# Performance work log

Hardware: AMD Instinct MI355X
Metric: run time of the kernel (lower is better)

The kernel has to match this reference:

```python
import jax, jax.numpy as jnp
import numpy as np

B, S, D = 512, 8, 1024
L = 6        # n_layers
LOOPS = 4    # n_loops
EPS = 1e-5   # LayerNorm eps (torch default)


def setup_inputs() -> dict:
    key = jax.random.key(0)
    ks = jax.random.split(key, 8)
    s = 1.0 / np.sqrt(D)  # torch Linear default init bound
    x = jax.random.normal(ks[0], (B, S, D), jnp.float32)
    gamma = jnp.ones((L, D), jnp.float32)
    beta = jnp.zeros((L, D), jnp.float32)
    Wg = jax.random.uniform(ks[1], (L, D, D), jnp.float32, -s, s)
    bg = jax.random.uniform(ks[2], (L, D), jnp.float32, -s, s)
    Wt = jax.random.uniform(ks[3], (L, D, D), jnp.float32, -s, s)
    bt = jax.random.uniform(ks[4], (L, D), jnp.float32, -s, s)
    Wc = jax.random.uniform(ks[5], (D, 1), jnp.float32, -s, s)
    bc = jax.random.uniform(ks[6], (1,), jnp.float32, -s, s)
    return {"x": x, "gamma": gamma, "beta": beta, "Wg": Wg, "bg": bg,
            "Wt": Wt, "bt": bt, "Wc": Wc, "bc": bc}


def _block(x, gamma, beta, Wg, bg, Wt, bt):
    # LayerNorm over last dim
    mu = jnp.mean(x, axis=-1, keepdims=True)
    var = jnp.mean(jnp.square(x - mu), axis=-1, keepdims=True)
    xn = (x - mu) * jax.lax.rsqrt(var + EPS) * gamma + beta
    g = jax.nn.sigmoid(jnp.einsum('bsd,de->bse', xn, Wg) + bg)
    t = jnp.tanh(jnp.einsum('bsd,de->bse', xn, Wt) + bt)
    return x * (1.0 - g) + t * g


def reference(x, gamma, beta, Wg, bg, Wt, bt, Wc, bc):
    confs = []
    for _ in range(LOOPS):
        for i in range(L):
            x = _block(x, gamma[i], beta[i], Wg[i], bg[i], Wt[i], bt[i])
        # confidence = sigmoid(Linear(x.mean(dim=1)))  -> (B, 1)
        confs.append(jax.nn.sigmoid(x.mean(axis=1) @ Wc + bc))
    return x, jnp.stack(confs)  # ((B,S,D), (LOOPS,B,1))
```

## Files before the change

### kernel.cpp

```cpp
#include <hip/hip_runtime.h>
#include <hip/hip_bf16.h>
#include <math.h>

#define B_ 512
#define S_ 8
#define D_ 1024
#define L_ 6
#define LOOPS_ 4
#define R_ (B_*S_)
#define LD_ (L_*D_)
#define EPSV 1e-5f

#define BM 128
#define BN 128
#define BK 64
#define NT (D_/BK)
#define TILE_USH 24576

typedef __attribute__((ext_vector_type(4))) float f32x4;
typedef __attribute__((ext_vector_type(8))) _Float16 f16x8;

__device__ __forceinline__ float bf2f(unsigned short u){
  union { float f; unsigned int i; } v; v.i = ((unsigned int)u) << 16; return v.f;
}
__device__ __forceinline__ unsigned short f2h(float f){
  _Float16 h = (_Float16)f;
  union { _Float16 h; unsigned short u; } v; v.h = h; return v.u;
}
__device__ __forceinline__ float loadf(const void* p, size_t i, int bf){
  return bf ? bf2f(((const unsigned short*)p)[i]) : ((const float*)p)[i];
}
__device__ __forceinline__ void gload16(const void* g, void* l){
  __builtin_amdgcn_global_load_lds((const __attribute__((address_space(1))) void*)g,
                                   (__attribute__((address_space(3))) void*)l, 16, 0, 0);
}

__global__ void k_detect(const unsigned int* __restrict__ gamma_raw, int* __restrict__ flag){
  if (threadIdx.x == 0 && blockIdx.x == 0)
    *flag = (gamma_raw[0] == 0x3F803F80u) ? 1 : 0;
}

__global__ void k_x2f(const void* __restrict__ x, float* __restrict__ xf,
                      const int* __restrict__ flag, int n4){
  int i = blockIdx.x * blockDim.x + threadIdx.x;
  if (i >= n4) return;
  if (*flag){
    ushort4 u = ((const ushort4*)x)[i];
    float4 f; f.x = bf2f(u.x); f.y = bf2f(u.y); f.z = bf2f(u.z); f.w = bf2f(u.w);
    ((float4*)xf)[i] = f;
  } else {
    ((float4*)xf)[i] = ((const float4*)x)[i];
  }
}

__global__ void k_small(const void* g, const void* b, const void* bgp, const void* btp,
                        const void* wcp, const void* bcp,
                        float* __restrict__ sm, const int* __restrict__ flag){
  int i = blockIdx.x * blockDim.x + threadIdx.x;
  int bf = *flag;
  if (i < LD_)               sm[i] = loadf(g,   i,          bf);
  else if (i < 2*LD_)        sm[i] = loadf(b,   i - LD_,    bf);
  else if (i < 3*LD_)        sm[i] = loadf(bgp, i - 2*LD_,  bf);
  else if (i < 4*LD_)        sm[i] = loadf(btp, i - 3*LD_,  bf);
  else if (i < 4*LD_ + D_)   sm[i] = loadf(wcp, i - 4*LD_,  bf);
  else if (i == 4*LD_ + D_)  sm[i] = loadf(bcp, 0,          bf);
}

__global__ void k_transpose(const void* __restrict__ Wg, const void* __restrict__ Wt,
                            ushort* __restrict__ WgT, ushort* __restrict__ WtT,
                            const int* __restrict__ flag){
  __shared__ ushort tile[32][33];
  int bf = *flag;
  int z = blockIdx.z;
  const void* src; ushort* dst;
  size_t base;
  if (z < L_) { src = Wg; dst = WgT + (size_t)z * D_ * D_;        base = (size_t)z * D_ * D_; }
  else        { src = Wt; dst = WtT + (size_t)(z - L_) * D_ * D_; base = (size_t)(z - L_) * D_ * D_; }
  int d0 = blockIdx.y * 32, e0 = blockIdx.x * 32;
  int tx = threadIdx.x, ty = threadIdx.y;
  #pragma unroll
  for (int i = 0; i < 4; i++){
    int r = ty + i * 8;
    size_t idx = base + (size_t)(d0 + r) * D_ + e0 + tx;
    float v = bf ? bf2f(((const ushort*)src)[idx]) : ((const float*)src)[idx];
    tile[r][tx] = f2h(v);
  }
  __syncthreads();
  #pragma unroll
  for (int i = 0; i < 4; i++){
    int r = ty + i * 8;
    dst[(size_t)(e0 + r) * D_ + d0 + tx] = tile[tx][r];
  }
}

__global__ __launch_bounds__(256) void k_ln(const float* __restrict__ xf,
            const float* __restrict__ gamma, const float* __restrict__ beta,
            ushort* __restrict__ xh){
  int w = threadIdx.x >> 6, lane = threadIdx.x & 63;
  int row = blockIdx.x * 4 + w;
  const float* xr = xf + (size_t)row * D_;
  float4 v[4];
  float s = 0.f, q = 0.f;
  #pragma unroll
  for (int p = 0; p < 4; p++){
    v[p] = *(const float4*)(xr + p * 256 + lane * 4);
    s += v[p].x + v[p].y + v[p].z + v[p].w;
    q += v[p].x * v[p].x + v[p].y * v[p].y + v[p].z * v[p].z + v[p].w * v[p].w;
  }
  #pragma unroll
  for (int o = 32; o; o >>= 1){ s += __shfl_xor(s, o); q += __shfl_xor(q, o); }
  float mu = s * (1.0f / D_);
  float var = q * (1.0f / D_) - mu * mu;
  float rs = rsqrtf(var + EPSV);
  #pragma unroll
  for (int p = 0; p < 4; p++){
    float4 g4 = *(const float4*)(gamma + p * 256 + lane * 4);
    float4 b4 = *(const float4*)(beta  + p * 256 + lane * 4);
    ushort4 o4;
    o4.x = f2h((v[p].x - mu) * rs * g4.x + b4.x);
    o4.y = f2h((v[p].y - mu) * rs * g4.y + b4.y);
    o4.z = f2h((v[p].z - mu) * rs * g4.z + b4.z);
    o4.w = f2h((v[p].w - mu) * rs * g4.w + b4.w);
    *(ushort4*)(xh + (size_t)row * D_ + p * 256 + lane * 4) = o4;
  }
}

__device__ __forceinline__ void stage_h0(const ushort* __restrict__ xh,
    const ushort* __restrict__ wg, ushort* __restrict__ buf,
    int mbase, int nbase, int kb, int w, int lane)
{
  int rr = lane >> 3;
  int clog = (lane & 7) ^ rr;
  int coff = kb + clog * 8;
  int r0 = w * 16;
  gload16(xh + (size_t)(mbase + r0 + rr)     * D_ + coff, buf + r0 * 64);
  gload16(xh + (size_t)(mbase + r0 + 8 + rr) * D_ + coff, buf + (r0 + 8) * 64);
  gload16(wg + (size_t)(nbase + r0 + rr)     * D_ + coff, buf + 8192 + r0 * 64);
}
__device__ __forceinline__ void stage_h1(const ushort* __restrict__ wg,
    const ushort* __restrict__ wt, ushort* __restrict__ buf,
    int nbase, int kb, int w, int lane)
{
  int rr = lane >> 3;
  int clog = (lane & 7) ^ rr;
  int coff = kb + clog * 8;
  int r0 = w * 16;
  gload16(wg + (size_t)(nbase + r0 + 8 + rr) * D_ + coff, buf + 8192 + (r0 + 8) * 64);
  gload16(wt + (size_t)(nbase + r0 + rr)     * D_ + coff, buf + 16384 + r0 * 64);
  gload16(wt + (size_t)(nbase + r0 + 8 + rr) * D_ + coff, buf + 16384 + (r0 + 8) * 64);
}

__global__ __launch_bounds__(512, 2) void k_gemm_gate(
    const ushort* __restrict__ xh,
    const ushort* __restrict__ WgT, const ushort* __restrict__ WtT,
    const float* __restrict__ bgf, const float* __restrict__ btf,
    float* __restrict__ xf)
{
  __shared__ __align__(16) ushort smem[3 * TILE_USH];

  const int t = threadIdx.x;
  const int lane = t & 63, w = t >> 6;
  const int wr = w >> 2, wn = w & 3;

  int bid = blockIdx.x;
  int swz = (bid & 7) * 32 + (bid >> 3);
  int mbase = (swz >> 3) * BM;
  int nbase = (swz & 7) * BN;

  f32x4 accg[4][2], acct[4][2];
  #pragma unroll
  for (int i = 0; i < 4; i++)
    #pragma unroll
    for (int j = 0; j < 2; j++){
      accg[i][j] = (f32x4){0.f, 0.f, 0.f, 0.f};
      acct[i][j] = (f32x4){0.f, 0.f, 0.f, 0.f};
    }

  stage_h0(xh, WgT, smem,            mbase, nbase, 0,  w, lane);
  stage_h1(WgT, WtT, smem,           nbase, 0,  w, lane);
  stage_h0(xh, WgT, smem + TILE_USH, mbase, nbase, BK, w, lane);
  stage_h1(WgT, WtT, smem + TILE_USH, nbase, BK, w, lane);
  asm volatile("s_waitcnt vmcnt(6)" ::: "memory");
  __builtin_amdgcn_s_barrier();

  for (int kt = 0; kt < NT; ++kt){
    ushort* cb = smem + (kt % 3) * TILE_USH;
    ushort* nb = smem + ((kt + 2) % 3) * TILE_USH;
    const bool doStage = (kt + 2 < NT);

    #pragma unroll
    for (int ks = 0; ks < 2; ++ks){
      int cl = ks * 4 + (lane >> 4);
      f16x8 af[4], bg2[2], bt2[2];
      #pragma unroll
      for (int mf = 0; mf < 4; mf++){
        int r = wr * 64 + mf * 16 + (lane & 15);
        af[mf] = *(const f16x8*)(cb + r * 64 + ((cl ^ (r & 7)) << 3));
      }
      #pragma unroll
      for (int nf = 0; nf < 2; nf++){
        int r = wn * 32 + nf * 16 + (lane & 15);
        int off = r * 64 + ((cl ^ (r & 7)) << 3);
        bg2[nf] = *(const f16x8*)(cb + 8192 + off);
        bt2[nf] = *(const f16x8*)(cb + 16384 + off);
      }
      if (doStage){
        if (ks == 0) stage_h0(xh, WgT, nb, mbase, nbase, (kt + 2) * BK, w, lane);
        else         stage_h1(WgT, WtT, nb, nbase, (kt + 2) * BK, w, lane);
      }
      __builtin_amdgcn_s_barrier();
      __builtin_amdgcn_s_setprio(1);
      #pragma unroll
      for (int mf = 0; mf < 4; mf++)
        #pragma unroll
        for (int nf = 0; nf < 2; nf++){
          accg[mf][nf] = __builtin_amdgcn_mfma_f32_16x16x32_f16(af[mf], bg2[nf], accg[mf][nf], 0, 0, 0);
          acct[mf][nf] = __builtin_amdgcn_mfma_f32_16x16x32_f16(af[mf], bt2[nf], acct[mf][nf], 0, 0, 0);
        }
      __builtin_amdgcn_s_setprio(0);
      if (ks == 1){
        if (kt == NT - 2)      asm volatile("s_waitcnt vmcnt(0)" ::: "memory");
        else if (kt < NT - 2)  asm volatile("s_waitcnt vmcnt(6)" ::: "memory");
      }
      __builtin_amdgcn_s_barrier();
    }
  }

  #pragma unroll
  for (int mf = 0; mf < 4; mf++){
    int row0 = mbase + wr * 64 + mf * 16 + ((lane >> 4) * 4);
    #pragma unroll
    for (int nf = 0; nf < 2; nf++){
      int col = nbase + wn * 32 + nf * 16 + (lane & 15);
      float bgv = bgf[col];
      float btv = btf[col];
      #pragma unroll
      for (int j = 0; j < 4; j++){
        float ug = accg[mf][nf][j] + bgv;
        float ut = acct[mf][nf][j] + btv;
        float g = 1.0f / (1.0f + expf(-ug));
        float tt = tanhf(ut);
        size_t idx = (size_t)(row0 + j) * D_ + col;
        float xo = xf[idx];
        xf[idx] = xo + g * (tt - xo);
      }
    }
  }
}

__global__ __launch_bounds__(256) void k_conf(const float* __restrict__ xf, const float* __restrict__ Wc,
                       const float* __restrict__ bc, float* __restrict__ out, int loop){
  int b = blockIdx.x;
  int t = threadIdx.x;
  const float* xb = xf + (size_t)b * S_ * D_;
  float acc = 0.f;
  for (int i = t; i < S_ * D_; i += 256){
    int d = i & (D_ - 1);
    acc += xb[i] * Wc[d];
  }
  #pragma unroll
  for (int o = 32; o; o >>= 1) acc += __shfl_xor(acc, o);
  __shared__ float wsum[4];
  int w = t >> 6, lane = t & 63;
  if (lane == 0) wsum[w] = acc;
  __syncthreads();
  if (t == 0){
    float s = wsum[0] + wsum[1] + wsum[2] + wsum[3];
    float z = s * (1.0f / S_) + bc[0];
    float c = 1.0f / (1.0f + expf(-z));
    out[(size_t)R_ * D_ + (size_t)loop * B_ + b] = c;
  }
}

__global__ void k_f2x(const float* __restrict__ xf, float* __restrict__ out, int n4){
  int i = blockIdx.x * blockDim.x + threadIdx.x;
  if (i >= n4) return;
  ((float4*)out)[i] = ((const float4*)xf)[i];
}

extern "C" void kernel_launch(void* const* d_in, const int* in_sizes, int n_in,
                              void* d_out, int out_size, void* d_ws, size_t ws_size,
                              hipStream_t stream){
  const void* x     = d_in[0];
  const void* gamma = d_in[1];
  const void* beta  = d_in[2];
  const void* Wg    = d_in[3];
  const void* bg    = d_in[4];
  const void* Wt    = d_in[5];
  const void* bt    = d_in[6];
  const void* Wc    = d_in[7];
  const void* bc    = d_in[8];
  float* out = (float*)d_out;

  char* ws = (char*)d_ws;
  float*  xf  = (float*)ws;
  ushort* xh  = (ushort*)(ws + (size_t)R_ * D_ * 4);
  ushort* WgT = xh + (size_t)R_ * D_;
  ushort* WtT = WgT + (size_t)L_ * D_ * D_;
  float*  sm  = (float*)(WtT + (size_t)L_ * D_ * D_);
  int*    flag = (int*)(sm + 4 * LD_ + D_ + 1);

  k_detect<<<1, 64, 0, stream>>>((const unsigned int*)gamma, flag);
  k_x2f<<<4096, 256, 0, stream>>>(x, xf, flag, R_ * D_ / 4);
  k_small<<<(4 * LD_ + D_ + 1 + 255) / 256, 256, 0, stream>>>(gamma, beta, bg, bt, Wc, bc, sm, flag);
  dim3 tb(32, 8); dim3 tg(D_ / 32, D_ / 32, 2 * L_);
  k_transpose<<<tg, tb, 0, stream>>>(Wg, Wt, WgT, WtT, flag);

  const float* smG  = sm;
  const float* smB  = sm + LD_;
  const float* smBg = sm + 2 * LD_;
  const float* smBt = sm + 3 * LD_;
  const float* smWc = sm + 4 * LD_;
  const float* smBc = sm + 4 * LD_ + D_;

  for (int loop = 0; loop < LOOPS_; ++loop){
    for (int l = 0; l < L_; ++l){
      k_ln<<<R_ / 4, 256, 0, stream>>>(xf, smG + (size_t)l * D_, smB + (size_t)l * D_, xh);
      k_gemm_gate<<<256, 512, 0, stream>>>(xh,
                                           WgT + (size_t)l * D_ * D_, WtT + (size_t)l * D_ * D_,
                                           smBg + (size_t)l * D_, smBt + (size_t)l * D_, xf);
    }
    k_conf<<<B_, 256, 0, stream>>>(xf, smWc, smBc, out, loop);
  }
  k_f2x<<<4096, 256, 0, stream>>>(xf, out, R_ * D_ / 4);
}
```

Measured before the change: 918.6 us.

## Fuse LayerNorm into gated GEMM by folding gamma/beta into weights and bias

Removes the separate LayerNorm kernel. Gamma is folded into the transposed fp16 weights and beta into precomputed biases (bias2 = b + beta·W). The GEMM kernel now computes per-row mean/rstd itself, reads fp32 x directly, normalizes and converts it to fp16 into LDS each k-step, and ping-pongs between two x buffers. This cuts the xh write/read round trip and a launch per layer, at the cost of extra fp32 A-operand loads, a stats prologue per block, and a restructured double-buffered pipeline.

```diff
diff --git a/kernel.cpp b/kernel.cpp
--- a/kernel.cpp
+++ b/kernel.cpp
@@ -15,7 +15,8 @@
 #define BN 128
 #define BK 64
 #define NT (D_/BK)
-#define TILE_USH 24576
+#define A_USH 8192
+#define B_USH 16384
 
 typedef __attribute__((ext_vector_type(4))) float f32x4;
 typedef __attribute__((ext_vector_type(8))) _Float16 f16x8;
@@ -26,6 +27,9 @@
 __device__ __forceinline__ unsigned short f2h(float f){
   _Float16 h = (_Float16)f;
   union { _Float16 h; unsigned short u; } v; v.h = h; return v.u;
+}
+__device__ __forceinline__ float h2f(unsigned short u){
+  union { unsigned short u; _Float16 h; } v; v.u = u; return (float)v.h;
 }
 __device__ __forceinline__ float loadf(const void* p, size_t i, int bf){
   return bf ? bf2f(((const unsigned short*)p)[i]) : ((const float*)p)[i];
@@ -68,14 +72,14 @@
 
 __global__ void k_transpose(const void* __restrict__ Wg, const void* __restrict__ Wt,
                             ushort* __restrict__ WgT, ushort* __restrict__ WtT,
-                            const int* __restrict__ flag){
+                            const float* __restrict__ sm, const int* __restrict__ flag){
   __shared__ ushort tile[32][33];
   int bf = *flag;
   int z = blockIdx.z;
-  const void* src; ushort* dst;
+  const void* src; ushort* dst; int lz;
   size_t base;
-  if (z < L_) { src = Wg; dst = WgT + (size_t)z * D_ * D_;        base = (size_t)z * D_ * D_; }
-  else        { src = Wt; dst = WtT + (size_t)(z - L_) * D_ * D_; base = (size_t)(z - L_) * D_ * D_; }
+  if (z < L_) { src = Wg; dst = WgT + (size_t)z * D_ * D_;        base = (size_t)z * D_ * D_; lz = z; }
+  else        { src = Wt; dst = WtT + (size_t)(z - L_) * D_ * D_; base = (size_t)(z - L_) * D_ * D_; lz = z - L_; }
   int d0 = blockIdx.y * 32, e0 = blockIdx.x * 32;
   int tx = threadIdx.x, ty = threadIdx.y;
   #pragma unroll
@@ -83,7 +87,8 @@
     int r = ty + i * 8;
     size_t idx = base + (size_t)(d0 + r) * D_ + e0 + tx;
     float v = bf ? bf2f(((const ushort*)src)[idx]) : ((const float*)src)[idx];
-    tile[r][tx] = f2h(v);
+    float gv = sm[(size_t)lz * D_ + d0 + r];
+    tile[r][tx] = f2h(gv * v);
   }
   __syncthreads();
   #pragma unroll
@@ -93,80 +98,73 @@
   }
 }
 
-__global__ __launch_bounds__(256) void k_ln(const float* __restrict__ xf,
-            const float* __restrict__ gamma, const float* __restrict__ beta,
-            ushort* __restrict__ xh){
-  int w = threadIdx.x >> 6, lane = threadIdx.x & 63;
-  int row = blockIdx.x * 4 + w;
-  const float* xr = xf + (size_t)row * D_;
-  float4 v[4];
-  float s = 0.f, q = 0.f;
-  #pragma unroll
-  for (int p = 0; p < 4; p++){
-    v[p] = *(const float4*)(xr + p * 256 + lane * 4);
-    s += v[p].x + v[p].y + v[p].z + v[p].w;
-    q += v[p].x * v[p].x + v[p].y * v[p].y + v[p].z * v[p].z + v[p].w * v[p].w;
-  }
-  #pragma unroll
-  for (int o = 32; o; o >>= 1){ s += __shfl_xor(s, o); q += __shfl_xor(q, o); }
-  float mu = s * (1.0f / D_);
-  float var = q * (1.0f / D_) - mu * mu;
-  float rs = rsqrtf(var + EPSV);
-  #pragma unroll
-  for (int p = 0; p < 4; p++){
-    float4 g4 = *(const float4*)(gamma + p * 256 + lane * 4);
-    float4 b4 = *(const float4*)(beta  + p * 256 + lane * 4);
-    ushort4 o4;
-    o4.x = f2h((v[p].x - mu) * rs * g4.x + b4.x);
-    o4.y = f2h((v[p].y - mu) * rs * g4.y + b4.y);
-    o4.z = f2h((v[p].z - mu) * rs * g4.z + b4.z);
-    o4.w = f2h((v[p].w - mu) * rs * g4.w + b4.w);
-    *(ushort4*)(xh + (size_t)row * D_ + p * 256 + lane * 4) = o4;
-  }
-}
-
-__device__ __forceinline__ void stage_h0(const ushort* __restrict__ xh,
-    const ushort* __restrict__ wg, ushort* __restrict__ buf,
-    int mbase, int nbase, int kb, int w, int lane)
+__global__ __launch_bounds__(256) void k_bias(const ushort* __restrict__ WgT, const ushort* __restrict__ WtT,
+                      const float* __restrict__ sm, float* __restrict__ bias2){
+  int idx = blockIdx.x * 256 + threadIdx.x;
+  int mat = idx / LD_;
+  int rem = idx - mat * LD_;
+  int l = rem >> 10, e = rem & 1023;
+  const ushort* WT = (mat ? WtT : WgT) + (size_t)l * D_ * D_ + (size_t)e * D_;
+  const float* beta = sm + LD_ + (size_t)l * D_;
+  float acc = sm[(size_t)(2 + mat) * LD_ + rem];
+  for (int d = 0; d < D_; d++)
+    acc += beta[d] * h2f(WT[d]);
+  bias2[idx] = acc;
+}
+
+__device__ __forceinline__ void stage_Bh(const ushort* __restrict__ wsrc,
+    ushort* __restrict__ dstbase, int nbase, int kb, int w, int lane)
 {
   int rr = lane >> 3;
   int clog = (lane & 7) ^ rr;
   int coff = kb + clog * 8;
   int r0 = w * 16;
-  gload16(xh + (size_t)(mbase + r0 + rr)     * D_ + coff, buf + r0 * 64);
-  gload16(xh + (size_t)(mbase + r0 + 8 + rr) * D_ + coff, buf + (r0 + 8) * 64);
-  gload16(wg + (size_t)(nbase + r0 + rr)     * D_ + coff, buf + 8192 + r0 * 64);
-}
-__device__ __forceinline__ void stage_h1(const ushort* __restrict__ wg,
-    const ushort* __restrict__ wt, ushort* __restrict__ buf,
-    int nbase, int kb, int w, int lane)
+  gload16(wsrc + (size_t)(nbase + r0 + rr) * D_ + coff,     dstbase + r0 * 64);
+  gload16(wsrc + (size_t)(nbase + r0 + 8 + rr) * D_ + coff, dstbase + (r0 + 8) * 64);
+}
+
+__global__ __launch_bounds__(512, 2) void k_gemm_gate(
+    const float* __restrict__ xin, float* __restrict__ xout,
+    const ushort* __restrict__ WgT, const ushort* __restrict__ WtT,
+    const float* __restrict__ bgf, const float* __restrict__ btf)
 {
-  int rr = lane >> 3;
-  int clog = (lane & 7) ^ rr;
-  int coff = kb + clog * 8;
-  int r0 = w * 16;
-  gload16(wg + (size_t)(nbase + r0 + 8 + rr) * D_ + coff, buf + 8192 + (r0 + 8) * 64);
-  gload16(wt + (size_t)(nbase + r0 + rr)     * D_ + coff, buf + 16384 + r0 * 64);
-  gload16(wt + (size_t)(nbase + r0 + 8 + rr) * D_ + coff, buf + 16384 + (r0 + 8) * 64);
-}
-
-__global__ __launch_bounds__(512, 2) void k_gemm_gate(
-    const ushort* __restrict__ xh,
-    const ushort* __restrict__ WgT, const ushort* __restrict__ WtT,
-    const float* __restrict__ bgf, const float* __restrict__ btf,
-    float* __restrict__ xf)
-{
-  __shared__ __align__(16) ushort smem[3 * TILE_USH];
+  __shared__ __align__(16) ushort smem[2 * A_USH + 3 * B_USH];
 
   const int t = threadIdx.x;
   const int lane = t & 63, w = t >> 6;
-  const int wr = w >> 2, wn = w & 3;
+  const int wrr = (w >> 2) * 64, wnn = (w & 3) * 32;
+  const int l15 = lane & 15;
 
   int bid = blockIdx.x;
   int swz = (bid & 7) * 32 + (bid >> 3);
   int mbase = (swz >> 3) * BM;
   int nbase = (swz & 7) * BN;
 
+  ushort* Abuf = smem;
+  ushort* Bbuf = smem + 2 * A_USH;
+
+  float mu = 0.f, rs = 0.f;
+  {
+    const float* xb = xin + (size_t)(mbase + w * 16) * D_;
+    for (int j = 0; j < 16; j++){
+      float s = 0.f, q = 0.f;
+      #pragma unroll
+      for (int p = 0; p < 4; p++){
+        float4 v = *(const float4*)(xb + (size_t)j * D_ + p * 256 + lane * 4);
+        s += v.x + v.y + v.z + v.w;
+        q += v.x * v.x + v.y * v.y + v.z * v.z + v.w * v.w;
+      }
+      #pragma unroll
+      for (int o = 32; o; o >>= 1){ s += __shfl_xor(s, o); q += __shfl_xor(q, o); }
+      float m = s * (1.0f / D_);
+      float r2 = rsqrtf(q * (1.0f / D_) - m * m + EPSV);
+      if ((lane >> 2) == j){ mu = m; rs = r2; }
+    }
+  }
+
+  const int ar = t >> 2, cq = t & 3;
+  const float* xrow = xin + (size_t)(mbase + ar) * D_;
+
   f32x4 accg[4][2], acct[4][2];
   #pragma unroll
   for (int i = 0; i < 4; i++)
@@ -176,62 +174,139 @@
       acct[i][j] = (f32x4){0.f, 0.f, 0.f, 0.f};
     }
 
-  stage_h0(xh, WgT, smem,            mbase, nbase, 0,  w, lane);
-  stage_h1(WgT, WtT, smem,           nbase, 0,  w, lane);
-  stage_h0(xh, WgT, smem + TILE_USH, mbase, nbase, BK, w, lane);
-  stage_h1(WgT, WtT, smem + TILE_USH, nbase, BK, w, lane);
-  asm volatile("s_waitcnt vmcnt(6)" ::: "memory");
+  float4 ra[4];
+  f16x8 af0[4], bg0[2], bt0[2];
+  f16x8 af1[4], bg1[2], bt1[2];
+
+  #pragma unroll
+  for (int i = 0; i < 2; i++)
+    #pragma unroll
+    for (int j = 0; j < 2; j++)
+      ra[i * 2 + j] = *(const float4*)(xrow + (cq + i * 4) * 8 + j * 4);
+  stage_Bh(WgT, Bbuf, nbase, 0, w, lane);
+  stage_Bh(WtT, Bbuf + 8192, nbase, 0, w, lane);
+  stage_Bh(WgT, Bbuf + B_USH, nbase, BK, w, lane);
+  stage_Bh(WtT, Bbuf + B_USH + 8192, nbase, BK, w, lane);
+  asm volatile("s_waitcnt vmcnt(8)" ::: "memory");
+  #pragma unroll
+  for (int i = 0; i < 2; i++){
+    int c = cq + i * 4;
+    float4 a0 = ra[i * 2], a1 = ra[i * 2 + 1];
+    f16x8 hv;
+    hv[0] = (_Float16)((a0.x - mu) * rs); hv[1] = (_Float16)((a0.y - mu) * rs);
+    hv[2] = (_Float16)((a0.z - mu) * rs); hv[3] = (_Float16)((a0.w - mu) * rs);
+    hv[4] = (_Float16)((a1.x - mu) * rs); hv[5] = (_Float16)((a1.y - mu) * rs);
+    hv[6] = (_Float16)((a1.z - mu) * rs); hv[7] = (_Float16)((a1.w - mu) * rs);
+    *(f16x8*)(Abuf + ar * 64 + ((c ^ (ar & 7)) << 3)) = hv;
+  }
+  asm volatile("s_waitcnt vmcnt(4)" ::: "memory");
   __builtin_amdgcn_s_barrier();
+  {
+    int cl = (lane >> 4);
+    #pragma unroll
+    for (int mf = 0; mf < 4; mf++){
+      int r = wrr + mf * 16 + l15;
+      af0[mf] = *(const f16x8*)(Abuf + r * 64 + ((cl ^ (r & 7)) << 3));
+    }
+    #pragma unroll
+    for (int nf = 0; nf < 2; nf++){
+      int r = wnn + nf * 16 + l15;
+      int off = r * 64 + ((cl ^ (r & 7)) << 3);
+      bg0[nf] = *(const f16x8*)(Bbuf + off);
+      bt0[nf] = *(const f16x8*)(Bbuf + 8192 + off);
+    }
+  }
 
   for (int kt = 0; kt < NT; ++kt){
-    ushort* cb = smem + (kt % 3) * TILE_USH;
-    ushort* nb = smem + ((kt + 2) % 3) * TILE_USH;
-    const bool doStage = (kt + 2 < NT);
-
-    #pragma unroll
-    for (int ks = 0; ks < 2; ++ks){
-      int cl = ks * 4 + (lane >> 4);
-      f16x8 af[4], bg2[2], bt2[2];
+    ushort* Ab = Abuf + (kt & 1) * A_USH;
+    ushort* An = Abuf + ((kt + 1) & 1) * A_USH;
+    ushort* Bb = Bbuf + (kt % 3) * B_USH;
+    ushort* Bn1 = Bbuf + ((kt + 1) % 3) * B_USH;
+    ushort* Bn2 = Bbuf + ((kt + 2) % 3) * B_USH;
+
+    {
+      int cl = 4 + (lane >> 4);
       #pragma unroll
       for (int mf = 0; mf < 4; mf++){
-        int r = wr * 64 + mf * 16 + (lane & 15);
-        af[mf] = *(const f16x8*)(cb + r * 64 + ((cl ^ (r & 7)) << 3));
+        int r = wrr + mf * 16 + l15;
+        af1[mf] = *(const f16x8*)(Ab + r * 64 + ((cl ^ (r & 7)) << 3));
       }
       #pragma unroll
       for (int nf = 0; nf < 2; nf++){
-        int r = wn * 32 + nf * 16 + (lane & 15);
+        int r = wnn + nf * 16 + l15;
         int off = r * 64 + ((cl ^ (r & 7)) << 3);
-        bg2[nf] = *(const f16x8*)(cb + 8192 + off);
-        bt2[nf] = *(const f16x8*)(cb + 16384 + off);
-      }
-      if (doStage){
-        if (ks == 0) stage_h0(xh, WgT, nb, mbase, nbase, (kt + 2) * BK, w, lane);
-        else         stage_h1(WgT, WtT, nb, nbase, (kt + 2) * BK, w, lane);
-      }
-      __builtin_amdgcn_s_barrier();
-      __builtin_amdgcn_s_setprio(1);
-      #pragma unroll
-      for (int mf = 0; mf < 4; mf++)
+        bg1[nf] = *(const f16x8*)(Bb + off);
+        bt1[nf] = *(const f16x8*)(Bb + 8192 + off);
+      }
+    }
+    if (kt + 1 < NT){
+      int kb = (kt + 1) * BK;
+      #pragma unroll
+      for (int i = 0; i < 2; i++)
         #pragma unroll
-        for (int nf = 0; nf < 2; nf++){
-          accg[mf][nf] = __builtin_amdgcn_mfma_f32_16x16x32_f16(af[mf], bg2[nf], accg[mf][nf], 0, 0, 0);
-          acct[mf][nf] = __builtin_amdgcn_mfma_f32_16x16x32_f16(af[mf], bt2[nf], acct[mf][nf], 0, 0, 0);
-        }
-      __builtin_amdgcn_s_setprio(0);
-      if (ks == 1){
-        if (kt == NT - 2)      asm volatile("s_waitcnt vmcnt(0)" ::: "memory");
-        else if (kt < NT - 2)  asm volatile("s_waitcnt vmcnt(6)" ::: "memory");
-      }
-      __builtin_amdgcn_s_barrier();
-    }
+        for (int j = 0; j < 2; j++)
+          ra[i * 2 + j] = *(const float4*)(xrow + kb + (cq + i * 4) * 8 + j * 4);
+    }
+    if (kt + 2 < NT) stage_Bh(WgT, Bn2, nbase, (kt + 2) * BK, w, lane);
+    __builtin_amdgcn_s_setprio(1);
+    #pragma unroll
+    for (int mf = 0; mf < 4; mf++)
+      #pragma unroll
+      for (int nf = 0; nf < 2; nf++){
+        accg[mf][nf] = __builtin_amdgcn_mfma_f32_16x16x32_f16(af0[mf], bg0[nf], accg[mf][nf], 0, 0, 0);
+        acct[mf][nf] = __builtin_amdgcn_mfma_f32_16x16x32_f16(af0[mf], bt0[nf], acct[mf][nf], 0, 0, 0);
+      }
+    __builtin_amdgcn_s_setprio(0);
+
+    if (kt + 2 < NT) stage_Bh(WtT, Bn2 + 8192, nbase, (kt + 2) * BK, w, lane);
+    if (kt + 1 < NT){
+      if (kt == NT - 2) asm volatile("s_waitcnt vmcnt(0)" ::: "memory");
+      else              asm volatile("s_waitcnt vmcnt(4)" ::: "memory");
+      #pragma unroll
+      for (int i = 0; i < 2; i++){
+        int c = cq + i * 4;
+        float4 a0 = ra[i * 2], a1 = ra[i * 2 + 1];
+        f16x8 hv;
+        hv[0] = (_Float16)((a0.x - mu) * rs); hv[1] = (_Float16)((a0.y - mu) * rs);
+        hv[2] = (_Float16)((a0.z - mu) * rs); hv[3] = (_Float16)((a0.w - mu) * rs);
+        hv[4] = (_Float16)((a1.x - mu) * rs); hv[5] = (_Float16)((a1.y - mu) * rs);
+        hv[6] = (_Float16)((a1.z - mu) * rs); hv[7] = (_Float16)((a1.w - mu) * rs);
+        *(f16x8*)(An + ar * 64 + ((c ^ (ar & 7)) << 3)) = hv;
+      }
+    }
+    __builtin_amdgcn_s_barrier();
+    if (kt + 1 < NT){
+      int cl = (lane >> 4);
+      #pragma unroll
+      for (int mf = 0; mf < 4; mf++){
+        int r = wrr + mf * 16 + l15;
+        af0[mf] = *(const f16x8*)(An + r * 64 + ((cl ^ (r & 7)) << 3));
+      }
+      #pragma unroll
+      for (int nf = 0; nf < 2; nf++){
+        int r = wnn + nf * 16 + l15;
+        int off = r * 64 + ((cl ^ (r & 7)) << 3);
+        bg0[nf] = *(const f16x8*)(Bn1 + off);
+        bt0[nf] = *(const f16x8*)(Bn1 + 8192 + off);
+      }
+    }
+    __builtin_amdgcn_s_setprio(1);
+    #pragma unroll
+    for (int mf = 0; mf < 4; mf++)
+      #pragma unroll
+      for (int nf = 0; nf < 2; nf++){
+        accg[mf][nf] = __builtin_amdgcn_mfma_f32_16x16x32_f16(af1[mf], bg1[nf], accg[mf][nf], 0, 0, 0);
+        acct[mf][nf] = __builtin_amdgcn_mfma_f32_16x16x32_f16(af1[mf], bt1[nf], acct[mf][nf], 0, 0, 0);
+      }
+    __builtin_amdgcn_s_setprio(0);
   }
 
   #pragma unroll
   for (int mf = 0; mf < 4; mf++){
-    int row0 = mbase + wr * 64 + mf * 16 + ((lane >> 4) * 4);
+    int row0 = mbase + wrr + mf * 16 + ((lane >> 4) * 4);
     #pragma unroll
     for (int nf = 0; nf < 2; nf++){
-      int col = nbase + wn * 32 + nf * 16 + (lane & 15);
+      int col = nbase + wnn + nf * 16 + l15;
       float bgv = bgf[col];
       float btv = btf[col];
       #pragma unroll
@@ -241,8 +316,8 @@
         float g = 1.0f / (1.0f + expf(-ug));
         float tt = tanhf(ut);
         size_t idx = (size_t)(row0 + j) * D_ + col;
-        float xo = xf[idx];
-        xf[idx] = xo + g * (tt - xo);
+        float xo = xin[idx];
+        xout[idx] = xo + g * (tt - xo);
       }
     }
   }
@@ -293,34 +368,34 @@
   float* out = (float*)d_out;
 
   char* ws = (char*)d_ws;
-  float*  xf  = (float*)ws;
-  ushort* xh  = (ushort*)(ws + (size_t)R_ * D_ * 4);
-  ushort* WgT = xh + (size_t)R_ * D_;
+  float*  xfA = (float*)ws;
+  float*  xfB = xfA + (size_t)R_ * D_;
+  ushort* WgT = (ushort*)(xfB + (size_t)R_ * D_);
   ushort* WtT = WgT + (size_t)L_ * D_ * D_;
   float*  sm  = (float*)(WtT + (size_t)L_ * D_ * D_);
-  int*    flag = (int*)(sm + 4 * LD_ + D_ + 1);
+  float*  bias2 = sm + 4 * LD_ + D_ + 1;
+  int*    flag  = (int*)(bias2 + 2 * LD_);
 
   k_detect<<<1, 64, 0, stream>>>((const unsigned int*)gamma, flag);
-  k_x2f<<<4096, 256, 0, stream>>>(x, xf, flag, R_ * D_ / 4);
   k_small<<<(4 * LD_ + D_ + 1 + 255) / 256, 256, 0, stream>>>(gamma, beta, bg, bt, Wc, bc, sm, flag);
+  k_x2f<<<4096, 256, 0, stream>>>(x, xfA, flag, R_ * D_ / 4);
   dim3 tb(32, 8); dim3 tg(D_ / 32, D_ / 32, 2 * L_);
-  k_transpose<<<tg, tb, 0, stream>>>(Wg, Wt, WgT, WtT, flag);
-
-  const float* smG  = sm;
-  const float* smB  = sm + LD_;
-  const float* smBg = sm + 2 * LD_;
-  const float* smBt = sm + 3 * LD_;
+  k_transpose<<<tg, tb, 0, stream>>>(Wg, Wt, WgT, WtT, sm, flag);
+  k_bias<<<2 * LD_ / 256, 256, 0, stream>>>(WgT, WtT, sm, bias2);
+
   const float* smWc = sm + 4 * LD_;
   const float* smBc = sm + 4 * LD_ + D_;
 
   for (int loop = 0; loop < LOOPS_; ++loop){
     for (int l = 0; l < L_; ++l){
-      k_ln<<<R_ / 4, 256, 0, stream>>>(xf, smG + (size_t)l * D_, smB + (size_t)l * D_, xh);
-      k_gemm_gate<<<256, 512, 0, stream>>>(xh,
+      int step = loop * L_ + l;
+      const float* xin = (step & 1) ? xfB : xfA;
+      float*       xo  = (step & 1) ? xfA : xfB;
+      k_gemm_gate<<<256, 512, 0, stream>>>(xin, xo,
                                            WgT + (size_t)l * D_ * D_, WtT + (size_t)l * D_ * D_,
-                                           smBg + (size_t)l * D_, smBt + (size_t)l * D_, xf);
-    }
-    k_conf<<<B_, 256, 0, stream>>>(xf, smWc, smBc, out, loop);
-  }
-  k_f2x<<<4096, 256, 0, stream>>>(xf, out, R_ * D_ / 4);
-}
+                                           bias2 + (size_t)l * D_, bias2 + (size_t)(L_ + l) * D_);
+    }
+    k_conf<<<B_, 256, 0, stream>>>(xfA, smWc, smBc, out, loop);
+  }
+  k_f2x<<<4096, 256, 0, stream>>>(xfA, out, R_ * D_ / 4);
+}
```

Result: slower. 1.060 ms (+15.4%).
